# Kernel tuning notes

Measured on AMD Instinct MI355X. Metric: run time of the kernel, lower is better.

The kernel has to match this reference:

```python
import jax, jax.numpy as jnp
import numpy as np

DIM = 1024
NUM_HEADS = 16
HEAD_DIM = 64
EPS = 1e-6

def setup_inputs() -> dict:
    key = jax.random.key(0)
    ks = jax.random.split(key, 6)
    x = jax.random.normal(ks[0], (4, 2048, DIM), dtype=jnp.float32)
    # Linear weights stored as (in, out); torch nn.Linear computes x @ W.T with W (out,in),
    # equivalent math with our (in,out) layout.
    Wq = jax.random.normal(ks[1], (DIM, NUM_HEADS * HEAD_DIM), dtype=jnp.float32) / np.sqrt(DIM)
    Wk = jax.random.normal(ks[2], (DIM, NUM_HEADS * HEAD_DIM), dtype=jnp.float32) / np.sqrt(DIM)
    Wv = jax.random.normal(ks[3], (DIM, NUM_HEADS * HEAD_DIM), dtype=jnp.float32) / np.sqrt(DIM)
    Wo = jax.random.normal(ks[4], (NUM_HEADS * HEAD_DIM, DIM), dtype=jnp.float32) / np.sqrt(NUM_HEADS * HEAD_DIM)
    # FeatureMap buffer: randn(head_dim, head_dim)/sqrt(head_dim)
    proj = jax.random.normal(ks[5], (HEAD_DIM, HEAD_DIM), dtype=jnp.float32) / np.sqrt(HEAD_DIM)
    return {"x": x, "Wq": Wq, "Wk": Wk, "Wv": Wv, "Wo": Wo, "proj": proj}

def _feature_map(x, proj):
    # phi(x) = elu(x @ proj) + 1  (positive features)
    return jax.nn.elu(x @ proj) + 1.0

def reference(x, Wq, Wk, Wv, Wo, proj):
    B, S, _ = x.shape
    H, D = NUM_HEADS, HEAD_DIM
    q = (x @ Wq).reshape(B, S, H, D)
    k = (x @ Wk).reshape(B, S, H, D)
    v = (x @ Wv).reshape(B, S, H, D)
    q = _feature_map(q, proj)
    k = _feature_map(k, proj)
    # scan over time: carry kv_state (B,H,D,D) and k_state (B,H,D)
    q_t = jnp.moveaxis(q, 1, 0)  # (S,B,H,D)
    k_t = jnp.moveaxis(k, 1, 0)
    v_t = jnp.moveaxis(v, 1, 0)

    def step(carry, qkv):
        kv, ksum = carry
        qt, kt, vt = qkv  # each (B,H,D)
        kv = kv + kt[..., :, None] * vt[..., None, :]  # outer product k v^T
        ksum = ksum + kt
        num = jnp.einsum('bhd,bhde->bhe', qt, kv)
        den = jnp.einsum('bhd,bhd->bh', qt, ksum) + EPS
        return (kv, ksum), num / den[..., None]

    kv0 = jnp.zeros((B, H, D, D), dtype=x.dtype)
    ks0 = jnp.zeros((B, H, D), dtype=x.dtype)
    _, out = jax.lax.scan(step, (kv0, ks0), (q_t, k_t, v_t))
    out = jnp.moveaxis(out, 0, 1).reshape(B, S, H * D)  # (B,S,H*D)
    return out @ Wo
```

## Files before the change

### kernel.cpp

```cpp
#include <hip/hip_runtime.h>

typedef unsigned short u16;
typedef unsigned int   u32;
typedef short bfrag8 __attribute__((ext_vector_type(8)));
typedef float facc4  __attribute__((ext_vector_type(4)));

#define DIM    1024
#define NH     16
#define HD     64
#define BSZ    4
#define SEQ    2048
#define MROWS  (BSZ*SEQ)
#define CHUNK  64
#define NCHUNK (SEQ/CHUNK)
#define BH     (BSZ*NH)
#define TS     72
#define NT     16

__device__ __forceinline__ u16 f2bf(float f) {
  u32 u = __builtin_bit_cast(u32, f);
  u32 r = u + 0x7fffu + ((u >> 16) & 1u);
  return (u16)(r >> 16);
}
__device__ __forceinline__ float bf2f(u16 b) {
  return __builtin_bit_cast(float, (u32)b << 16);
}

__device__ __forceinline__ void gload_lds16(const void* g, void* l) {
  __builtin_amdgcn_global_load_lds((const __attribute__((address_space(1))) u32*)g,
                                   (__attribute__((address_space(3))) u32*)l, 16, 0, 0);
}


__global__ __launch_bounds__(256) void conv_f32_bf16(const float* __restrict__ in, u16* __restrict__ out) {
  const int i = (blockIdx.x * 256 + threadIdx.x) * 4;
  const float4 v = *(const float4*)(in + i);
  ushort4 o;
  o.x = f2bf(v.x); o.y = f2bf(v.y); o.z = f2bf(v.z); o.w = f2bf(v.w);
  *(ushort4*)(out + i) = o;
}

__global__ __launch_bounds__(256) void fold_qk(const float* __restrict__ Wq, const float* __restrict__ Wk,
                                               const float* __restrict__ proj, u16* __restrict__ wt) {
  const int i0 = blockIdx.x * 32;
  const int h  = blockIdx.y;
  const int sel = blockIdx.z;
  const float* W = sel ? Wk : Wq;
  u16* out = wt + (size_t)sel * (DIM*DIM);
  __shared__ float sp[64*64];
  __shared__ float sw[32*64];
  const int tid = threadIdx.x;
  for (int idx = tid; idx < 4096; idx += 256) sp[idx] = proj[idx];
  for (int idx = tid; idx < 2048; idx += 256) {
    int r = idx >> 6, c = idx & 63;
    sw[idx] = W[(size_t)(i0 + r)*DIM + h*64 + c];
  }
  __syncthreads();
  const int i  = tid >> 3;
  const int e0 = (tid & 7) * 8;
  #pragma unroll
  for (int ee = 0; ee < 8; ++ee) {
    const int e = e0 + ee;
    float acc = 0.f;
    for (int d = 0; d < 64; ++d) acc += sw[i*64 + d] * sp[d*64 + e];
    out[(size_t)(h*64 + e)*DIM + i0 + i] = f2bf(acc);
  }
}

__global__ __launch_bounds__(256) void trans_conv(const float* __restrict__ Wv, const float* __restrict__ Wo,
                                                  u16* __restrict__ wt) {
  const int sel = blockIdx.z;
  const float* in = sel ? Wo : Wv;
  u16* out = wt + (size_t)(2 + sel) * (DIM*DIM);
  const int n0 = blockIdx.x * 32, k0 = blockIdx.y * 32;
  __shared__ float tile[32][33];
  const int tid = threadIdx.x;
  for (int idx = tid; idx < 1024; idx += 256) {
    int r = idx >> 5, c = idx & 31;
    tile[r][c] = in[(size_t)(k0 + r)*DIM + n0 + c];
  }
  __syncthreads();
  for (int idx = tid; idx < 1024; idx += 256) {
    int r = idx >> 5, c = idx & 31;
    out[(size_t)(n0 + r)*DIM + k0 + c] = f2bf(tile[c][r]);
  }
}


#define PH_OPEN() { asm volatile("s_barrier" ::: "memory"); __builtin_amdgcn_sched_barrier(0); \
                    __builtin_amdgcn_s_setprio(1); }
#define PH_CLOSE(VM) { __builtin_amdgcn_s_setprio(0); __builtin_amdgcn_sched_barrier(0); \
                       asm volatile("s_waitcnt vmcnt(" #VM ")" ::: "memory"); \
                       asm volatile("s_barrier" ::: "memory"); }
#define PH_CLOSE0() { __builtin_amdgcn_s_setprio(0); __builtin_amdgcn_sched_barrier(0); \
                      asm volatile("s_barrier" ::: "memory"); }

#define SU(mat, rb, kt, dstbase, seg) \
  gload_lds16((mat) + (size_t)((rb) + (seg)*64 + (tid>>3))*DIM + (kt)*64 + ((((tid)&7) ^ ((tid>>3)&7)) << 3), \
              (dstbase) + (seg)*4096 + tid*8);

#define RDX01(dst, XB) { _Pragma("unroll") for(int mf=0;mf<2;++mf){ _Pragma("unroll") for(int kh=0;kh<2;++kh){ \
  const int row = wm*64 + mf*16 + lr; \
  dst[mf*2+kh] = *(const bfrag8*)&(XB)[row*64 + (((kh*4+g) ^ (row&7)) << 3)]; } } }
#define RDX23(dst, XB) { _Pragma("unroll") for(int mf=0;mf<2;++mf){ _Pragma("unroll") for(int kh=0;kh<2;++kh){ \
  const int row = wm*64 + (2+mf)*16 + lr; \
  dst[mf*2+kh] = *(const bfrag8*)&(XB)[row*64 + (((kh*4+g) ^ (row&7)) << 3)]; } } }
#define RDW01(dst, WB) { _Pragma("unroll") for(int nf=0;nf<2;++nf){ _Pragma("unroll") for(int kh=0;kh<2;++kh){ \
  const int row = wn*32 + nf*16 + lr; \
  dst[nf*2+kh] = *(const bfrag8*)&(WB)[row*64 + (((kh*4+g) ^ (row&7)) << 3)]; } } }
#define RDW23(dst, WB) { _Pragma("unroll") for(int nf=0;nf<2;++nf){ _Pragma("unroll") for(int kh=0;kh<2;++kh){ \
  const int row = 128 + wn*32 + nf*16 + lr; \
  dst[nf*2+kh] = *(const bfrag8*)&(WB)[row*64 + (((kh*4+g) ^ (row&7)) << 3)]; } } }

#define MMQ(NHh, MHh, XF, WF) { \
  _Pragma("unroll") for(int nf=0;nf<2;++nf){ _Pragma("unroll") for(int mf=0;mf<2;++mf){ \
  _Pragma("unroll") for(int kh=0;kh<2;++kh){ \
    acc[(NHh)*2+nf][(MHh)*2+mf] = __builtin_amdgcn_mfma_f32_16x16x32_bf16( \
        WF[nf*2+kh], XF[mf*2+kh], acc[(NHh)*2+nf][(MHh)*2+mf], 0, 0, 0); } } } }

template<int MODE>
__global__ __launch_bounds__(512, 1)
void gemmR(const u16* __restrict__ A, const u16* __restrict__ W,
           u16* __restrict__ outb, float* __restrict__ outf) {
  __shared__ u16 lds[3*8192 + 3*16384];
  u16* ldsX = lds;
  u16* ldsW = lds + 3*8192;
  const int tid  = threadIdx.x;
  const int wave = tid >> 6, lane = tid & 63;
  const int wm = wave >> 2, wn = wave & 3;
  const int lr = lane & 15, g = lane >> 4;

  const int NY  = (MODE == 0) ? 12 : 4;
  const int q   = (int)gridDim.x >> 3;
  const int bid = (int)blockIdx.x;
  const int nf_ = (bid & 7) * q + (bid >> 3);
  const int m0  = (nf_ / NY) * 128;
  const int ngl = (nf_ % NY) * 256;

  SU(A, m0, 0, ldsX, 0);            SU(A, m0, 0, ldsX, 1);
  SU(W, ngl, 0, ldsW, 0);           SU(W, ngl, 0, ldsW, 1);
  SU(W, ngl, 0, ldsW, 2);           SU(W, ngl, 0, ldsW, 3);
  SU(A, m0, 1, ldsX + 8192, 0);     SU(A, m0, 1, ldsX + 8192, 1);
  SU(W, ngl, 1, ldsW + 16384, 0);   SU(W, ngl, 1, ldsW + 16384, 1);
  SU(W, ngl, 1, ldsW + 16384, 2);   SU(W, ngl, 1, ldsW + 16384, 3);
  asm volatile("s_waitcnt vmcnt(6)" ::: "memory");
  asm volatile("s_barrier" ::: "memory");

  facc4 acc[4][4] = {};
  bfrag8 xf01a[4], xf23a[4], wf01a[4], wf23a[4];
  bfrag8 xf01b[4], xf23b[4], wf01b[4], wf23b[4];

  RDX01(xf01a, ldsX); RDW01(wf01a, ldsW);

  int bE = 0, bO = 1, bS = 2;
  for (int p = 0; p < 7; ++p) {
    const int E = 2*p;
    const u16* xbE = ldsX + bE*8192;   u16* xbEm = ldsX + bE*8192;
    const u16* wbE = ldsW + bE*16384;  u16* wbEm = ldsW + bE*16384;
    const u16* xbO = ldsX + bO*8192;
    const u16* wbO = ldsW + bO*16384;
    u16* xbS = ldsX + bS*8192;
    u16* wbS = ldsW + bS*16384;
    RDX23(xf23a, xbE); SU(A, m0, E+2, xbS, 0); SU(A, m0, E+2, xbS, 1);
    PH_OPEN(); MMQ(0,0,xf01a,wf01a); PH_CLOSE(8);
    RDW23(wf23a, wbE); SU(W, ngl, E+2, wbS, 0); SU(W, ngl, E+2, wbS, 1);
    PH_OPEN(); MMQ(0,1,xf23a,wf01a); PH_CLOSE(8);
    RDX01(xf01b, xbO); SU(W, ngl, E+2, wbS, 2); SU(W, ngl, E+2, wbS, 3);
    PH_OPEN(); MMQ(1,0,xf01a,wf23a); PH_CLOSE(8);
    RDW01(wf01b, wbO);
    PH_OPEN(); MMQ(1,1,xf23a,wf23a); PH_CLOSE0();
    RDX23(xf23b, xbO); SU(A, m0, E+3, xbEm, 0); SU(A, m0, E+3, xbEm, 1);
    PH_OPEN(); MMQ(0,0,xf01b,wf01b); PH_CLOSE(8);
    RDW23(wf23b, wbO); SU(W, ngl, E+3, wbEm, 0); SU(W, ngl, E+3, wbEm, 1);
    PH_OPEN(); MMQ(0,1,xf23b,wf01b); PH_CLOSE(8);
    RDX01(xf01a, xbS); SU(W, ngl, E+3, wbEm, 2); SU(W, ngl, E+3, wbEm, 3);
    PH_OPEN(); MMQ(1,0,xf01b,wf23b); PH_CLOSE(8);
    RDW01(wf01a, wbS);
    PH_OPEN(); MMQ(1,1,xf23b,wf23b); PH_CLOSE0();
    const int t_ = bE; bE = bS; bS = bO; bO = t_;
  }
  {
    const u16* xbE = ldsX + bE*8192;
    const u16* wbE = ldsW + bE*16384;
    const u16* xbO = ldsX + bO*8192;
    const u16* wbO = ldsW + bO*16384;
    RDX23(xf23a, xbE);
    PH_OPEN(); MMQ(0,0,xf01a,wf01a); PH_CLOSE(6);
    RDW23(wf23a, wbE);
    PH_OPEN(); MMQ(0,1,xf23a,wf01a); PH_CLOSE(4);
    RDX01(xf01b, xbO);
    PH_OPEN(); MMQ(1,0,xf01a,wf23a); PH_CLOSE(2);
    RDW01(wf01b, wbO);
    PH_OPEN(); MMQ(1,1,xf23a,wf23a); PH_CLOSE0();
    RDX23(xf23b, xbO);
    PH_OPEN(); MMQ(0,0,xf01b,wf01b); PH_CLOSE(0);
    RDW23(wf23b, wbO);
    PH_OPEN(); MMQ(0,1,xf23b,wf01b); PH_CLOSE0();
    PH_OPEN(); MMQ(1,0,xf01b,wf23b); PH_CLOSE0();
    PH_OPEN(); MMQ(1,1,xf23b,wf23b);
    __builtin_amdgcn_s_setprio(0);
  }

  const int sel = (MODE == 0) ? (ngl >> 10) : 0;
  const bool doElu = (MODE == 0) && (sel < 2);
  const int coly = (MODE == 0) ? (ngl & 1023) : ngl;
  #pragma unroll
  for (int nh = 0; nh < 2; ++nh) {
    #pragma unroll
    for (int nf = 0; nf < 2; ++nf) {
      #pragma unroll
      for (int mf = 0; mf < 4; ++mf) {
        const facc4 a = acc[nh*2+nf][mf];
        const int m = m0 + wm*64 + mf*16 + lr;
        const int col0 = coly + nh*128 + wn*32 + nf*16 + g*4;
        float v0 = a[0], v1 = a[1], v2 = a[2], v3 = a[3];
        if (MODE == 0) {
          if (doElu) {
            v0 = (v0 > 0.f) ? (v0 + 1.f) : __expf(v0);
            v1 = (v1 > 0.f) ? (v1 + 1.f) : __expf(v1);
            v2 = (v2 > 0.f) ? (v2 + 1.f) : __expf(v2);
            v3 = (v3 > 0.f) ? (v3 + 1.f) : __expf(v3);
          }
          uint2 pk;
          pk.x = (u32)f2bf(v0) | ((u32)f2bf(v1) << 16);
          pk.y = (u32)f2bf(v2) | ((u32)f2bf(v3) << 16);
          *(uint2*)&outb[(size_t)sel*((size_t)MROWS*DIM) + (size_t)m*DIM + col0] = pk;
        } else {
          float4 pk; pk.x = v0; pk.y = v1; pk.z = v2; pk.w = v3;
          *(float4*)&outf[(size_t)m*DIM + col0] = pk;
        }
      }
    }
  }
}


__global__ __launch_bounds__(256) void phaseA(const u16* __restrict__ Kb, const u16* __restrict__ Vb,
                                              u16* __restrict__ Ast, float* __restrict__ ksum) {
  const int c = blockIdx.x, bh = blockIdx.y;
  const int b = bh >> 4, h = bh & 15;
  const int tid = threadIdx.x;
  const int wave = tid >> 6, lane = tid & 63, lr = lane & 15, g = lane >> 4;
  __shared__ u16 lKt[64*TS];
  __shared__ u16 lVt[64*TS];
  const size_t mbase = (size_t)b*SEQ + (size_t)c*CHUNK;

  for (int s = tid; s < 512; s += 256) {
    const int t = s >> 3, dg = (s & 7) * 8;
    const bfrag8 kk = *(const bfrag8*)&Kb[(mbase + t)*DIM + h*64 + dg];
    const bfrag8 vv = *(const bfrag8*)&Vb[(mbase + t)*DIM + h*64 + dg];
    #pragma unroll
    for (int j = 0; j < 8; ++j) {
      lKt[(dg + j)*TS + t] = (u16)kk[j];
      lVt[(dg + j)*TS + t] = (u16)vv[j];
    }
  }
  __syncthreads();

  facc4 acc[4] = {};
  #pragma unroll
  for (int kt = 0; kt < 2; ++kt) {
    const bfrag8 af = *(const bfrag8*)&lVt[(wave*16 + lr)*TS + kt*32 + g*8];
    #pragma unroll
    for (int j = 0; j < 4; ++j) {
      const bfrag8 bk = *(const bfrag8*)&lKt[(j*16 + lr)*TS + kt*32 + g*8];
      acc[j] = __builtin_amdgcn_mfma_f32_16x16x32_bf16(af, bk, acc[j], 0, 0, 0);
    }
  }
  u16* dst = Ast + (((size_t)bh*NCHUNK + c) << 12);
  #pragma unroll
  for (int j = 0; j < 4; ++j)
    #pragma unroll
    for (int r = 0; r < 4; ++r)
      dst[(wave*16 + g*4 + r)*64 + j*16 + lr] = f2bf(acc[j][r]);

  const int d = tid >> 2, seg = tid & 3;
  const bfrag8 k0 = *(const bfrag8*)&lKt[d*TS + seg*16];
  const bfrag8 k1 = *(const bfrag8*)&lKt[d*TS + seg*16 + 8];
  float s = 0.f;
  #pragma unroll
  for (int j = 0; j < 8; ++j) s += bf2f((u16)k0[j]) + bf2f((u16)k1[j]);
  s += __shfl_xor(s, 1, 64);
  s += __shfl_xor(s, 2, 64);
  if (seg == 0) ksum[((size_t)bh*NCHUNK + c)*64 + d] = s;
}

__global__ __launch_bounds__(256) void phaseB(u16* __restrict__ Ast, float* __restrict__ ksum) {
  const int bh = blockIdx.x, slice = blockIdx.y;
  const int tid = threadIdx.x;
  u16* base = Ast + (size_t)bh*NCHUNK*4096 + slice*256 + tid;
  float v[NCHUNK];
  #pragma unroll
  for (int c = 0; c < NCHUNK; ++c) v[c] = bf2f(base[(size_t)c*4096]);
  float run = 0.f;
  #pragma unroll
  for (int c = 0; c < NCHUNK; ++c) { base[(size_t)c*4096] = f2bf(run); run += v[c]; }
  if (slice == 0 && tid < 64) {
    float rs = 0.f;
    float* kp = ksum + (size_t)bh*NCHUNK*64 + tid;
    for (int c = 0; c < NCHUNK; ++c) { const float t = kp[c*64]; kp[c*64] = rs; rs += t; }
  }
}

__global__ __launch_bounds__(256) void phaseC(const u16* __restrict__ Qb, const u16* __restrict__ Kb,
                                              const u16* __restrict__ Vb, const u16* __restrict__ Ast,
                                              const float* __restrict__ ksum, u16* __restrict__ Ob) {
  const int c = blockIdx.x, bh = blockIdx.y;
  const int b = bh >> 4, h = bh & 15;
  const int tid = threadIdx.x;
  const int wave = tid >> 6, lane = tid & 63, lr = lane & 15, g = lane >> 4;
  __shared__ u16 lS  [64*TS];
  __shared__ u16 lVt [64*TS];
  __shared__ u16 lKVt[64*TS];
  __shared__ float lks[64];
  __shared__ float lrs[64];
  __shared__ float lqk[64];
  const size_t mbase = (size_t)b*SEQ + (size_t)c*CHUNK;

  for (int s = tid; s < 512; s += 256) {
    const int t = s >> 3, dg = (s & 7) * 8;
    const bfrag8 vv = *(const bfrag8*)&Vb[(mbase + t)*DIM + h*64 + dg];
    #pragma unroll
    for (int j = 0; j < 8; ++j) lVt[(dg + j)*TS + t] = (u16)vv[j];
  }
  const u16* kvsrc = Ast + (((size_t)bh*NCHUNK + c) << 12);
  for (int s = tid; s < 512; s += 256) {
    const int e = s >> 3, dg = (s & 7) * 8;
    *(bfrag8*)&lKVt[e*TS + dg] = *(const bfrag8*)&kvsrc[e*64 + dg];
  }
  if (tid < 64) lks[tid] = ksum[((size_t)bh*NCHUNK + c)*64 + tid];

  bfrag8 qf[2], kf[4][2];
  {
    const u16* qrow = Qb + (mbase + wave*16 + lr)*DIM + h*64;
    qf[0] = *(const bfrag8*)&qrow[g*8];
    qf[1] = *(const bfrag8*)&qrow[32 + g*8];
  }
  #pragma unroll
  for (int j = 0; j < 4; ++j) {
    const u16* krow = Kb + (mbase + j*16 + lr)*DIM + h*64;
    kf[j][0] = *(const bfrag8*)&krow[g*8];
    kf[j][1] = *(const bfrag8*)&krow[32 + g*8];
  }

  facc4 accs[4] = {};
  #pragma unroll
  for (int kt = 0; kt < 2; ++kt)
    #pragma unroll
    for (int j = 0; j < 4; ++j)
      accs[j] = __builtin_amdgcn_mfma_f32_16x16x32_bf16(qf[kt], kf[j][kt], accs[j], 0, 0, 0);

  float rs[4] = {0.f, 0.f, 0.f, 0.f};
  #pragma unroll
  for (int j = 0; j < 4; ++j) {
    const int cc = j*16 + lr;
    #pragma unroll
    for (int r = 0; r < 4; ++r) {
      const int rr = wave*16 + g*4 + r;
      const float vS = (cc <= rr) ? accs[j][r] : 0.f;
      rs[r] += vS;
      lS[rr*TS + cc] = f2bf(vS);
    }
  }
  #pragma unroll
  for (int r = 0; r < 4; ++r) {
    float t = rs[r];
    t += __shfl_xor(t, 1, 64); t += __shfl_xor(t, 2, 64);
    t += __shfl_xor(t, 4, 64); t += __shfl_xor(t, 8, 64);
    if (lr == 0) lrs[wave*16 + g*4 + r] = t;
  }
  __syncthreads();

  {
    const u16* qr2 = Qb + (mbase + wave*16 + lr)*DIM + h*64 + g*16;
    const bfrag8 a0 = *(const bfrag8*)&qr2[0];
    const bfrag8 a1 = *(const bfrag8*)&qr2[8];
    float t = 0.f;
    #pragma unroll
    for (int j = 0; j < 8; ++j)
      t += bf2f((u16)a0[j]) * lks[g*16 + j] + bf2f((u16)a1[j]) * lks[g*16 + 8 + j];
    t += __shfl_xor(t, 16, 64);
    t += __shfl_xor(t, 32, 64);
    if (g == 0) lqk[wave*16 + lr] = t;
  }

  facc4 acco[4] = {};
  #pragma unroll
  for (int kt = 0; kt < 2; ++kt) {
    const bfrag8 sf = *(const bfrag8*)&lS[(wave*16 + lr)*TS + kt*32 + g*8];
    #pragma unroll
    for (int j = 0; j < 4; ++j) {
      const bfrag8 vf = *(const bfrag8*)&lVt[(j*16 + lr)*TS + kt*32 + g*8];
      acco[j] = __builtin_amdgcn_mfma_f32_16x16x32_bf16(sf, vf, acco[j], 0, 0, 0);
    }
  }
  #pragma unroll
  for (int kt = 0; kt < 2; ++kt)
    #pragma unroll
    for (int j = 0; j < 4; ++j) {
      const bfrag8 kvf = *(const bfrag8*)&lKVt[(j*16 + lr)*TS + kt*32 + g*8];
      acco[j] = __builtin_amdgcn_mfma_f32_16x16x32_bf16(qf[kt], kvf, acco[j], 0, 0, 0);
    }

  #pragma unroll
  for (int r = 0; r < 4; ++r) {
    const int rr = wave*16 + g*4 + r;
    const float rden = 1.0f / (lrs[rr] + lqk[rr] + 1e-6f);
    #pragma unroll
    for (int j = 0; j < 4; ++j)
      Ob[(mbase + rr)*DIM + h*64 + j*16 + lr] = f2bf(acco[j][r] * rden);
  }
}

extern "C" void kernel_launch(void* const* d_in, const int* in_sizes, int n_in,
                              void* d_out, int out_size, void* d_ws, size_t ws_size,
                              hipStream_t stream) {
  const float* x    = (const float*)d_in[0];
  const float* Wq   = (const float*)d_in[1];
  const float* Wk   = (const float*)d_in[2];
  const float* Wv   = (const float*)d_in[3];
  const float* Wo   = (const float*)d_in[4];
  const float* proj = (const float*)d_in[5];
  float* out = (float*)d_out;

  char* ws = (char*)d_ws;
  u16*   xb   = (u16*)  (ws);
  u16*   wt   = (u16*)  (ws + 16777216);
  u16*   qkv  = (u16*)  (ws + 25165824);
  u16*   Ob   = (u16*)  (ws + 75497472);
  u16*   Ast  = (u16*)  (ws + 92274688);
  float* ksum = (float*)(ws + 109051904);
  (void)ws_size; (void)in_sizes; (void)n_in; (void)out_size;

  conv_f32_bf16<<<dim3((MROWS*DIM)/1024), 256, 0, stream>>>(x, xb);
  fold_qk      <<<dim3(DIM/32, NH, 2), 256, 0, stream>>>(Wq, Wk, proj, wt);
  trans_conv   <<<dim3(DIM/32, DIM/32, 2), 256, 0, stream>>>(Wv, Wo, wt);

  gemmR<0><<<dim3(64*12), 512, 0, stream>>>(xb, wt, qkv, nullptr);

  const u16* Qb = qkv;
  const u16* Kb = qkv + (size_t)MROWS*DIM;
  const u16* Vb = qkv + 2*(size_t)MROWS*DIM;

  phaseA<<<dim3(NCHUNK, BH), 256, 0, stream>>>(Kb, Vb, Ast, ksum);
  phaseB<<<dim3(BH, 16), 256, 0, stream>>>(Ast, ksum);
  phaseC<<<dim3(NCHUNK, BH), 256, 0, stream>>>(Qb, Kb, Vb, Ast, ksum, Ob);

  gemmR<1><<<dim3(64*4), 512, 0, stream>>>(Ob, wt + 3*(size_t)DIM*DIM, nullptr, out);
}
```

Measured before the change: 189.5 us.

## Restructure GEMM main loop into two half-phases per K-tile with fewer barriers

Reworks the software-pipelined bf16 MFMA GEMM so that each K-tile is computed in two half phases, each covering all four M fragments for one half of N, instead of four quarter phases. The old code had a barrier on both sides of every quarter. The new schedule has one barrier in the middle of each tile and one at its end, plus explicit lgkmcnt waits. All eight X fragments are read at once and the global-to-LDS loads for the next stages are regrouped. The aim is to cut barrier count and synchronisation overhead and to give longer uninterrupted MFMA runs. The cost is higher fragment register pressure and different vmcnt wait thresholds, which could expose load latency or create LDS hazards.

Result: faster. 185.0 us (-2.3%).

```diff
diff --git a/kernel.cpp b/kernel.cpp
--- a/kernel.cpp
+++ b/kernel.cpp
@@ -87,40 +87,36 @@
 }
 
 
-#define PH_OPEN() { asm volatile("s_barrier" ::: "memory"); __builtin_amdgcn_sched_barrier(0); \
-                    __builtin_amdgcn_s_setprio(1); }
-#define PH_CLOSE(VM) { __builtin_amdgcn_s_setprio(0); __builtin_amdgcn_sched_barrier(0); \
-                       asm volatile("s_waitcnt vmcnt(" #VM ")" ::: "memory"); \
-                       asm volatile("s_barrier" ::: "memory"); }
-#define PH_CLOSE0() { __builtin_amdgcn_s_setprio(0); __builtin_amdgcn_sched_barrier(0); \
-                      asm volatile("s_barrier" ::: "memory"); }
+#define SBAR0() __builtin_amdgcn_sched_barrier(0)
+#define OPA()   { asm volatile("s_waitcnt lgkmcnt(0)" ::: "memory"); SBAR0(); }
+#define MID(VM) { SBAR0(); asm volatile("s_waitcnt vmcnt(" #VM ")" ::: "memory"); \
+                  asm volatile("s_barrier" ::: "memory"); }
+#define ENDB()  { SBAR0(); asm volatile("s_barrier" ::: "memory"); }
 
 #define SU(mat, rb, kt, dstbase, seg) \
   gload_lds16((mat) + (size_t)((rb) + (seg)*64 + (tid>>3))*DIM + (kt)*64 + ((((tid)&7) ^ ((tid>>3)&7)) << 3), \
               (dstbase) + (seg)*4096 + tid*8);
 
-#define RDX01(dst, XB) { _Pragma("unroll") for(int mf=0;mf<2;++mf){ _Pragma("unroll") for(int kh=0;kh<2;++kh){ \
+#define RD_X8(dst, XB) { _Pragma("unroll") for(int mf=0;mf<4;++mf){ _Pragma("unroll") for(int kh=0;kh<2;++kh){ \
   const int row = wm*64 + mf*16 + lr; \
   dst[mf*2+kh] = *(const bfrag8*)&(XB)[row*64 + (((kh*4+g) ^ (row&7)) << 3)]; } } }
-#define RDX23(dst, XB) { _Pragma("unroll") for(int mf=0;mf<2;++mf){ _Pragma("unroll") for(int kh=0;kh<2;++kh){ \
-  const int row = wm*64 + (2+mf)*16 + lr; \
-  dst[mf*2+kh] = *(const bfrag8*)&(XB)[row*64 + (((kh*4+g) ^ (row&7)) << 3)]; } } }
-#define RDW01(dst, WB) { _Pragma("unroll") for(int nf=0;nf<2;++nf){ _Pragma("unroll") for(int kh=0;kh<2;++kh){ \
+#define RD_W01(dst, WB) { _Pragma("unroll") for(int nf=0;nf<2;++nf){ _Pragma("unroll") for(int kh=0;kh<2;++kh){ \
   const int row = wn*32 + nf*16 + lr; \
   dst[nf*2+kh] = *(const bfrag8*)&(WB)[row*64 + (((kh*4+g) ^ (row&7)) << 3)]; } } }
-#define RDW23(dst, WB) { _Pragma("unroll") for(int nf=0;nf<2;++nf){ _Pragma("unroll") for(int kh=0;kh<2;++kh){ \
+#define RD_W23(dst, WB) { _Pragma("unroll") for(int nf=0;nf<2;++nf){ _Pragma("unroll") for(int kh=0;kh<2;++kh){ \
   const int row = 128 + wn*32 + nf*16 + lr; \
   dst[nf*2+kh] = *(const bfrag8*)&(WB)[row*64 + (((kh*4+g) ^ (row&7)) << 3)]; } } }
 
-#define MMQ(NHh, MHh, XF, WF) { \
-  _Pragma("unroll") for(int nf=0;nf<2;++nf){ _Pragma("unroll") for(int mf=0;mf<2;++mf){ \
+#define MMH(NHh, WF, XF) { __builtin_amdgcn_s_setprio(1); \
+  _Pragma("unroll") for(int nf=0;nf<2;++nf){ _Pragma("unroll") for(int mf=0;mf<4;++mf){ \
   _Pragma("unroll") for(int kh=0;kh<2;++kh){ \
-    acc[(NHh)*2+nf][(MHh)*2+mf] = __builtin_amdgcn_mfma_f32_16x16x32_bf16( \
-        WF[nf*2+kh], XF[mf*2+kh], acc[(NHh)*2+nf][(MHh)*2+mf], 0, 0, 0); } } } }
+    acc[(NHh)*2+nf][mf] = __builtin_amdgcn_mfma_f32_16x16x32_bf16( \
+        WF[nf*2+kh], XF[mf*2+kh], acc[(NHh)*2+nf][mf], 0, 0, 0); } } } \
+  __builtin_amdgcn_s_setprio(0); }
 
 template<int MODE>
 __global__ __launch_bounds__(512, 1)
-void gemmR(const u16* __restrict__ A, const u16* __restrict__ W,
+void gemmP(const u16* __restrict__ A, const u16* __restrict__ W,
            u16* __restrict__ outb, float* __restrict__ outf) {
   __shared__ u16 lds[3*8192 + 3*16384];
   u16* ldsX = lds;
@@ -147,58 +143,61 @@
   asm volatile("s_barrier" ::: "memory");
 
   facc4 acc[4][4] = {};
-  bfrag8 xf01a[4], xf23a[4], wf01a[4], wf23a[4];
-  bfrag8 xf01b[4], xf23b[4], wf01b[4], wf23b[4];
-
-  RDX01(xf01a, ldsX); RDW01(wf01a, ldsW);
+  bfrag8 xfa[8], w01a[4], w23a[4];
+  bfrag8 xfb[8], w01b[4], w23b[4];
+
+  RD_X8(xfa, ldsX); RD_W01(w01a, ldsW);
 
   int bE = 0, bO = 1, bS = 2;
   for (int p = 0; p < 7; ++p) {
     const int E = 2*p;
-    const u16* xbE = ldsX + bE*8192;   u16* xbEm = ldsX + bE*8192;
-    const u16* wbE = ldsW + bE*16384;  u16* wbEm = ldsW + bE*16384;
-    const u16* xbO = ldsX + bO*8192;
-    const u16* wbO = ldsW + bO*16384;
-    u16* xbS = ldsX + bS*8192;
-    u16* wbS = ldsW + bS*16384;
-    RDX23(xf23a, xbE); SU(A, m0, E+2, xbS, 0); SU(A, m0, E+2, xbS, 1);
-    PH_OPEN(); MMQ(0,0,xf01a,wf01a); PH_CLOSE(8);
-    RDW23(wf23a, wbE); SU(W, ngl, E+2, wbS, 0); SU(W, ngl, E+2, wbS, 1);
-    PH_OPEN(); MMQ(0,1,xf23a,wf01a); PH_CLOSE(8);
-    RDX01(xf01b, xbO); SU(W, ngl, E+2, wbS, 2); SU(W, ngl, E+2, wbS, 3);
-    PH_OPEN(); MMQ(1,0,xf01a,wf23a); PH_CLOSE(8);
-    RDW01(wf01b, wbO);
-    PH_OPEN(); MMQ(1,1,xf23a,wf23a); PH_CLOSE0();
-    RDX23(xf23b, xbO); SU(A, m0, E+3, xbEm, 0); SU(A, m0, E+3, xbEm, 1);
-    PH_OPEN(); MMQ(0,0,xf01b,wf01b); PH_CLOSE(8);
-    RDW23(wf23b, wbO); SU(W, ngl, E+3, wbEm, 0); SU(W, ngl, E+3, wbEm, 1);
-    PH_OPEN(); MMQ(0,1,xf23b,wf01b); PH_CLOSE(8);
-    RDX01(xf01a, xbS); SU(W, ngl, E+3, wbEm, 2); SU(W, ngl, E+3, wbEm, 3);
-    PH_OPEN(); MMQ(1,0,xf01b,wf23b); PH_CLOSE(8);
-    RDW01(wf01a, wbS);
-    PH_OPEN(); MMQ(1,1,xf23b,wf23b); PH_CLOSE0();
+    u16* xE = ldsX + bE*8192;   u16* wE = ldsW + bE*16384;
+    u16* xO = ldsX + bO*8192;   u16* wO = ldsW + bO*16384;
+    u16* xS = ldsX + bS*8192;   u16* wS = ldsW + bS*16384;
+    OPA();
+    RD_W23(w23a, wE);
+    SU(A, m0, E+2, xS, 0); SU(A, m0, E+2, xS, 1);
+    SBAR0();
+    MMH(0, w01a, xfa);
+    MID(2);
+    RD_X8(xfb, xO); RD_W01(w01b, wO);
+    SU(W, ngl, E+2, wS, 0); SU(W, ngl, E+2, wS, 1);
+    SU(W, ngl, E+2, wS, 2); SU(W, ngl, E+2, wS, 3);
+    SBAR0();
+    MMH(1, w23a, xfa);
+    ENDB();
+    OPA();
+    RD_W23(w23b, wO);
+    SU(A, m0, E+3, xE, 0); SU(A, m0, E+3, xE, 1);
+    SBAR0();
+    MMH(0, w01b, xfb);
+    MID(2);
+    RD_X8(xfa, xS); RD_W01(w01a, wS);
+    SU(W, ngl, E+3, wE, 0); SU(W, ngl, E+3, wE, 1);
+    SU(W, ngl, E+3, wE, 2); SU(W, ngl, E+3, wE, 3);
+    SBAR0();
+    MMH(1, w23b, xfb);
+    ENDB();
     const int t_ = bE; bE = bS; bS = bO; bO = t_;
   }
   {
-    const u16* xbE = ldsX + bE*8192;
-    const u16* wbE = ldsW + bE*16384;
-    const u16* xbO = ldsX + bO*8192;
-    const u16* wbO = ldsW + bO*16384;
-    RDX23(xf23a, xbE);
-    PH_OPEN(); MMQ(0,0,xf01a,wf01a); PH_CLOSE(6);
-    RDW23(wf23a, wbE);
-    PH_OPEN(); MMQ(0,1,xf23a,wf01a); PH_CLOSE(4);
-    RDX01(xf01b, xbO);
-    PH_OPEN(); MMQ(1,0,xf01a,wf23a); PH_CLOSE(2);
-    RDW01(wf01b, wbO);
-    PH_OPEN(); MMQ(1,1,xf23a,wf23a); PH_CLOSE0();
-    RDX23(xf23b, xbO);
-    PH_OPEN(); MMQ(0,0,xf01b,wf01b); PH_CLOSE(0);
-    RDW23(wf23b, wbO);
-    PH_OPEN(); MMQ(0,1,xf23b,wf01b); PH_CLOSE0();
-    PH_OPEN(); MMQ(1,0,xf01b,wf23b); PH_CLOSE0();
-    PH_OPEN(); MMQ(1,1,xf23b,wf23b);
-    __builtin_amdgcn_s_setprio(0);
+    u16* wE = ldsW + bE*16384;
+    u16* xO = ldsX + bO*8192;   u16* wO = ldsW + bO*16384;
+    OPA();
+    RD_W23(w23a, wE);
+    SBAR0();
+    MMH(0, w01a, xfa);
+    MID(0);
+    RD_X8(xfb, xO); RD_W01(w01b, wO);
+    SBAR0();
+    MMH(1, w23a, xfa);
+    ENDB();
+    OPA();
+    RD_W23(w23b, wO);
+    SBAR0();
+    MMH(0, w01b, xfb);
+    ENDB();
+    MMH(1, w23b, xfb);
   }
 
   const int sel = (MODE == 0) ? (ngl >> 10) : 0;
@@ -436,7 +435,7 @@
   fold_qk      <<<dim3(DIM/32, NH, 2), 256, 0, stream>>>(Wq, Wk, proj, wt);
   trans_conv   <<<dim3(DIM/32, DIM/32, 2), 256, 0, stream>>>(Wv, Wo, wt);
 
-  gemmR<0><<<dim3(64*12), 512, 0, stream>>>(xb, wt, qkv, nullptr);
+  gemmP<0><<<dim3(64*12), 512, 0, stream>>>(xb, wt, qkv, nullptr);
 
   const u16* Qb = qkv;
   const u16* Kb = qkv + (size_t)MROWS*DIM;
@@ -446,5 +445,5 @@
   phaseB<<<dim3(BH, 16), 256, 0, stream>>>(Ast, ksum);
   phaseC<<<dim3(NCHUNK, BH), 256, 0, stream>>>(Qb, Kb, Vb, Ast, ksum, Ob);
 
-  gemmR<1><<<dim3(64*4), 512, 0, stream>>>(Ob, wt + 3*(size_t)DIM*DIM, nullptr, out);
-}
+  gemmP<1><<<dim3(64*4), 512, 0, stream>>>(Ob, wt + 3*(size_t)DIM*DIM, nullptr, out);
+}
```
